# Optimization experiments

Measured on AMD Instinct MI355X. Metric: run time of the kernel, lower is better.

The kernel has to match this reference:

```python
import jax, jax.numpy as jnp
import numpy as np

V, C, H, L, T, B = 256, 1024, 16, 6, 1024, 8
HS = C // H
EPS = 1e-5


def setup_inputs() -> dict:
    key = jax.random.key(0)
    ks = jax.random.split(key, 20)
    s = 0.02
    inp = {
        "idx": jax.random.randint(ks[0], (B, T), 0, V),
        "tok_emb": jax.random.normal(ks[1], (V, C), jnp.float32) * s,
        "pos_emb": jax.random.normal(ks[2], (T, C), jnp.float32) * s,
        "Wq": jax.random.normal(ks[3], (L, C, C), jnp.float32) * s,
        "Wk": jax.random.normal(ks[4], (L, C, C), jnp.float32) * s,
        "Wv": jax.random.normal(ks[5], (L, C, C), jnp.float32) * s,
        "Wo": jax.random.normal(ks[6], (L, C, C), jnp.float32) * s,
        "bo": jnp.zeros((L, C), jnp.float32),
        "ln1_g": jnp.ones((L, C), jnp.float32),
        "ln1_b": jnp.zeros((L, C), jnp.float32),
        "ln2_g": jnp.ones((L, C), jnp.float32),
        "ln2_b": jnp.zeros((L, C), jnp.float32),
        "W1": jax.random.normal(ks[7], (L, C, 4 * C), jnp.float32) * s,
        "b1": jnp.zeros((L, 4 * C), jnp.float32),
        "W2": jax.random.normal(ks[8], (L, 4 * C, C), jnp.float32) * s,
        "b2": jnp.zeros((L, C), jnp.float32),
        "lnf_g": jnp.ones((C,), jnp.float32),
        "lnf_b": jnp.zeros((C,), jnp.float32),
        "Whead": jax.random.normal(ks[9], (C, V), jnp.float32) * s,
        "bhead": jnp.zeros((V,), jnp.float32),
    }
    return inp


def _ln(x, g, b):
    mu = jnp.mean(x, axis=-1, keepdims=True)
    var = jnp.mean(jnp.square(x - mu), axis=-1, keepdims=True)
    return (x - mu) * jax.lax.rsqrt(var + EPS) * g + b


def reference(idx, tok_emb, pos_emb, Wq, Wk, Wv, Wo, bo, ln1_g, ln1_b,
              ln2_g, ln2_b, W1, b1, W2, b2, lnf_g, lnf_b, Whead, bhead):
    Bv, Tv = idx.shape
    x = tok_emb[idx] + pos_emb[:Tv]  # [B,T,C]
    causal = jnp.tril(jnp.ones((Tv, Tv), bool))  # [T,T]
    scale = 1.0 / np.sqrt(HS)
    neg_inf = jnp.finfo(x.dtype).min
    for l in range(L):
        h = _ln(x, ln1_g[l], ln1_b[l])
        q = (h @ Wq[l]).reshape(Bv, Tv, H, HS)
        k = (h @ Wk[l]).reshape(Bv, Tv, H, HS)
        v = (h @ Wv[l]).reshape(Bv, Tv, H, HS)
        wei = jnp.einsum("bthd,bshd->bhts", q, k) * scale  # [B,H,T,T]
        wei = jnp.where(causal, wei, neg_inf)
        wei = jax.nn.softmax(wei, axis=-1)
        att = jnp.einsum("bhts,bshd->bthd", wei, v).reshape(Bv, Tv, C)
        x = x + att @ Wo[l] + bo[l]
        h2 = _ln(x, ln2_g[l], ln2_b[l])
        x = x + jax.nn.relu(h2 @ W1[l] + b1[l]) @ W2[l] + b2[l]
    x = _ln(x, lnf_g, lnf_b)
    logits = x @ Whead + bhead  # [B,T,V]
    return logits
```

## Files before the change

### kernel.cpp

```cpp
#include <hip/hip_runtime.h>

typedef unsigned short u16;
typedef unsigned int   u32;
typedef __attribute__((ext_vector_type(4))) float  f32x4;
typedef __attribute__((ext_vector_type(8))) __bf16 bf16x8;
typedef __attribute__((ext_vector_type(8))) short  s16x8;
typedef __attribute__((ext_vector_type(4))) unsigned short u16x4;

#define DEVFN __device__ __forceinline__

DEVFN float bf2f(u16 u) {
    u32 v = ((u32)u) << 16;
    return __builtin_bit_cast(float, v);
}
DEVFN u16 f2bf(float f) {
    u32 u = __builtin_bit_cast(u32, f);
    u32 r = u + 0x7FFFu + ((u >> 16) & 1u);
    return (u16)(r >> 16);
}

DEVFN void gload16(const void* g, void* l) {
    __builtin_amdgcn_global_load_lds(
        (const __attribute__((address_space(1))) void*)g,
        (__attribute__((address_space(3))) void*)l, 16, 0, 0);
}

__global__ __launch_bounds__(256) void embed_k(const int* __restrict__ idx,
                                               const float* __restrict__ tok,
                                               const float* __restrict__ pos,
                                               float* __restrict__ x)
{
    int i   = blockIdx.x * 256 + threadIdx.x;
    int row = i >> 8;
    int c   = (i & 255) << 2;
    int t   = row & 1023;
    int tk  = idx[row];
    float4 a = *(const float4*)&tok[(size_t)tk * 1024 + c];
    float4 p = *(const float4*)&pos[(size_t)t * 1024 + c];
    float4 r; r.x = a.x + p.x; r.y = a.y + p.y; r.z = a.z + p.z; r.w = a.w + p.w;
    *(float4*)&x[(size_t)row * 1024 + c] = r;
}

__global__ __launch_bounds__(256) void transpose_k(const float* __restrict__ W,
                                                   u16* __restrict__ Wt, int K, int N)
{
    __shared__ float tile[32][33];
    int n0 = blockIdx.x * 32, k0 = blockIdx.y * 32;
    int xx = threadIdx.x, ty = threadIdx.y;
#pragma unroll
    for (int yy = 0; yy < 4; ++yy) {
        int y = ty + yy * 8;
        tile[y][xx] = W[(size_t)(k0 + y) * N + n0 + xx];
    }
    __syncthreads();
#pragma unroll
    for (int yy = 0; yy < 4; ++yy) {
        int y = ty + yy * 8;
        Wt[(size_t)(n0 + y) * K + k0 + xx] = f2bf(tile[xx][y]);
    }
}

__global__ __launch_bounds__(256) void ln_k(const float* __restrict__ x,
                                            const float* __restrict__ g,
                                            const float* __restrict__ b,
                                            u16* __restrict__ out)
{
    const int row = blockIdx.x, tid = threadIdx.x;
    const float4 v = *(const float4*)&x[(size_t)row * 1024 + tid * 4];
    __shared__ float red[8];
    float s = v.x + v.y + v.z + v.w;
#pragma unroll
    for (int off = 32; off > 0; off >>= 1) s += __shfl_down(s, off);
    const int lane = tid & 63, wv = tid >> 6;
    if (lane == 0) red[wv] = s;
    __syncthreads();
    const float mu = (red[0] + red[1] + red[2] + red[3]) * (1.0f / 1024.0f);
    const float dx = v.x - mu, dy = v.y - mu, dz = v.z - mu, dw = v.w - mu;
    float s2 = dx * dx + dy * dy + dz * dz + dw * dw;
#pragma unroll
    for (int off = 32; off > 0; off >>= 1) s2 += __shfl_down(s2, off);
    if (lane == 0) red[4 + wv] = s2;
    __syncthreads();
    const float var = (red[4] + red[5] + red[6] + red[7]) * (1.0f / 1024.0f);
    const float rs  = rsqrtf(var + 1e-5f);
    const float4 gv = *(const float4*)&g[tid * 4];
    const float4 bv = *(const float4*)&b[tid * 4];
    u16x4 o;
    o.x = f2bf(dx * rs * gv.x + bv.x);
    o.y = f2bf(dy * rs * gv.y + bv.y);
    o.z = f2bf(dz * rs * gv.z + bv.z);
    o.w = f2bf(dw * rs * gv.w + bv.w);
    *(u16x4*)&out[(size_t)row * 1024 + tid * 4] = o;
}

template <int MODE>
__global__ __launch_bounds__(256) void gemm_bt(const u16* __restrict__ A,
                                               const u16* __restrict__ Bt,
                                               const float* __restrict__ bias,
                                               float* __restrict__ RES,
                                               u16* __restrict__ Ob,
                                               float* __restrict__ Of,
                                               int N, int K)
{
    __shared__ __align__(16) u16 As[128 * 32];
    __shared__ __align__(16) u16 Bs[128 * 32];
    const int tid  = threadIdx.x;
    const int lane = tid & 63, wave = tid >> 6;
    const int wr = wave >> 1, wc = wave & 1;
    const int l15 = lane & 15, l4 = lane >> 4;
    const int m0 = blockIdx.y * 128, n0 = blockIdx.x * 128;

    f32x4 acc[4][4];
    const f32x4 zz = {0.f, 0.f, 0.f, 0.f};
#pragma unroll
    for (int i = 0; i < 4; ++i)
#pragma unroll
        for (int j = 0; j < 4; ++j) acc[i][j] = zz;

    const int r0 = tid >> 2, q0q = (tid & 3) * 8;
    const int r1 = (tid + 256) >> 2, q1q = ((tid + 256) & 3) * 8;

    for (int k0 = 0; k0 < K; k0 += 32) {
        gload16(&A [(size_t)(m0 + r0) * K + k0 + q0q], &As[tid * 8]);
        gload16(&Bt[(size_t)(n0 + r0) * K + k0 + q0q], &Bs[tid * 8]);
        gload16(&A [(size_t)(m0 + r1) * K + k0 + q1q], &As[(tid + 256) * 8]);
        gload16(&Bt[(size_t)(n0 + r1) * K + k0 + q1q], &Bs[(tid + 256) * 8]);
        __syncthreads();
        s16x8 af[4], bw[4];
#pragma unroll
        for (int i = 0; i < 4; ++i)
            af[i] = *(const s16x8*)&As[(wr * 64 + i * 16 + l15) * 32 + l4 * 8];
#pragma unroll
        for (int j = 0; j < 4; ++j)
            bw[j] = *(const s16x8*)&Bs[(wc * 64 + j * 16 + l15) * 32 + l4 * 8];
#pragma unroll
        for (int i = 0; i < 4; ++i)
#pragma unroll
            for (int j = 0; j < 4; ++j)
                acc[i][j] = __builtin_amdgcn_mfma_f32_16x16x32_bf16(
                    __builtin_bit_cast(bf16x8, af[i]),
                    __builtin_bit_cast(bf16x8, bw[j]), acc[i][j], 0, 0, 0);
        __syncthreads();
    }

#pragma unroll
    for (int i = 0; i < 4; ++i) {
        const int rb = m0 + wr * 64 + i * 16 + l4 * 4;
#pragma unroll
        for (int j = 0; j < 4; ++j) {
            const int col = n0 + wc * 64 + j * 16 + l15;
            const float bval = (MODE == 0) ? 0.0f : bias[col];
#pragma unroll
            for (int r = 0; r < 4; ++r) {
                const size_t o = (size_t)(rb + r) * N + col;
                const float v = acc[i][j][r];
                if (MODE == 0)      Ob[o] = f2bf(v);
                else if (MODE == 1) RES[o] += v + bval;
                else if (MODE == 2) Ob[o] = f2bf(fmaxf(v + bval, 0.0f));
                else                Of[o] = v + bval;
            }
        }
    }
}

__global__ __launch_bounds__(256) void attn_mfma_k(const u16* __restrict__ QKV,
                                                   u16* __restrict__ Og)
{
    const int qt  = (int)(gridDim.x - 1 - blockIdx.x);
    const int bh  = blockIdx.y;
    const int b   = bh >> 4, h = bh & 15;
    const int tid = threadIdx.x;
    const int wq  = tid >> 6, lane = tid & 63;
    const int l15 = lane & 15, l4 = lane >> 4;

    __shared__ __align__(16) u16 Ks[64][72];
    __shared__ __align__(16) u16 Vt[64][72];
    __shared__ __align__(16) u16 Ps[4][16][68];
    u32* VtW = (u32*)&Vt[0][0];

    const int qrow0 = qt * 128 + wq * 32;

    const u16* Qbase = QKV + (size_t)b * 1024 * 3072 + h * 64;
    const u16* Kbase = Qbase + 1024;
    const u16* Vbase = Qbase + 2048;

    s16x8 aQ[2][2];
#pragma unroll
    for (int qi = 0; qi < 2; ++qi) {
        const u16* qsrc = Qbase + (size_t)(qrow0 + qi * 16 + l15) * 3072;
        aQ[qi][0] = *(const s16x8*)(qsrc + l4 * 8);
        aQ[qi][1] = *(const s16x8*)(qsrc + 32 + l4 * 8);
    }

    f32x4 O[2][4];
    const f32x4 zz = {0.f, 0.f, 0.f, 0.f};
    float mrow[2][4], lrow[2][4];
#pragma unroll
    for (int qi = 0; qi < 2; ++qi) {
#pragma unroll
        for (int dj = 0; dj < 4; ++dj) O[qi][dj] = zz;
#pragma unroll
        for (int r = 0; r < 4; ++r) { mrow[qi][r] = -3.0e38f; lrow[qi][r] = 0.f; }
    }

    const int srow = tid >> 3;
    const int soff = (tid & 7) * 8;
    const int vp   = tid >> 3;
    const int vdg  = tid & 7;

    const int ntiles = 2 * qt + 2;
    for (int t = 0; t < ntiles; ++t) {
        const int kv0 = t * 64;
        __syncthreads();
        {
            const u16* kb0 = Kbase + (size_t)(kv0 + srow) * 3072 + soff;
            *(s16x8*)&Ks[srow][soff]      = *(const s16x8*)kb0;
            *(s16x8*)&Ks[srow + 32][soff] = *(const s16x8*)(kb0 + (size_t)32 * 3072);
        }
        {
            const u16* vb0 = Vbase + (size_t)(kv0 + 2 * vp) * 3072 + vdg * 8;
            s16x8 v0 = *(const s16x8*)vb0;
            s16x8 v1 = *(const s16x8*)(vb0 + 3072);
#pragma unroll
            for (int e = 0; e < 8; ++e) {
                const int d = vdg * 8 + e;
                const int c = (vp + 4 * vdg) & 31;
                u32 pk = (u32)(u16)v0[e] | ((u32)(u16)v1[e] << 16);
                VtW[d * 36 + c] = pk;
            }
        }
        __syncthreads();

#pragma unroll
        for (int qi = 0; qi < 2; ++qi) {
            const int qlo = qrow0 + qi * 16;
            if (kv0 > qlo + 15) continue;
            f32x4 S[4];
#pragma unroll
            for (int kc = 0; kc < 4; ++kc) {
                f32x4 s = zz;
                s16x8 bK0 = *(const s16x8*)&Ks[kc * 16 + l15][l4 * 8];
                s16x8 bK1 = *(const s16x8*)&Ks[kc * 16 + l15][32 + l4 * 8];
                s = __builtin_amdgcn_mfma_f32_16x16x32_bf16(
                    __builtin_bit_cast(bf16x8, aQ[qi][0]), __builtin_bit_cast(bf16x8, bK0), s, 0, 0, 0);
                s = __builtin_amdgcn_mfma_f32_16x16x32_bf16(
                    __builtin_bit_cast(bf16x8, aQ[qi][1]), __builtin_bit_cast(bf16x8, bK1), s, 0, 0, 0);
#pragma unroll
                for (int r = 0; r < 4; ++r) S[kc][r] = s[r] * 0.125f;
            }
            if (kv0 + 63 > qlo) {
#pragma unroll
                for (int kc = 0; kc < 4; ++kc) {
                    const int k = kv0 + kc * 16 + l15;
#pragma unroll
                    for (int r = 0; r < 4; ++r)
                        if (k > qlo + l4 * 4 + r) S[kc][r] = -3.0e38f;
                }
            }
            float mloc[4];
#pragma unroll
            for (int r = 0; r < 4; ++r)
                mloc[r] = fmaxf(fmaxf(S[0][r], S[1][r]), fmaxf(S[2][r], S[3][r]));
#pragma unroll
            for (int off = 1; off < 16; off <<= 1)
#pragma unroll
                for (int r = 0; r < 4; ++r) mloc[r] = fmaxf(mloc[r], __shfl_xor(mloc[r], off));
            float alpha[4];
#pragma unroll
            for (int r = 0; r < 4; ++r) {
                const float mnew = fmaxf(mrow[qi][r], mloc[r]);
                alpha[r] = __expf(mrow[qi][r] - mnew);
                mrow[qi][r] = mnew;
            }
            float psum[4] = {0.f, 0.f, 0.f, 0.f};
#pragma unroll
            for (int kc = 0; kc < 4; ++kc)
#pragma unroll
                for (int r = 0; r < 4; ++r) {
                    const float p = __expf(S[kc][r] - mrow[qi][r]);
                    Ps[wq][l4 * 4 + r][kc * 16 + l15] = f2bf(p);
                    psum[r] += p;
                }
#pragma unroll
            for (int off = 1; off < 16; off <<= 1)
#pragma unroll
                for (int r = 0; r < 4; ++r) psum[r] += __shfl_xor(psum[r], off);
#pragma unroll
            for (int r = 0; r < 4; ++r) lrow[qi][r] = lrow[qi][r] * alpha[r] + psum[r];
#pragma unroll
            for (int dj = 0; dj < 4; ++dj)
#pragma unroll
                for (int r = 0; r < 4; ++r) O[qi][dj][r] *= alpha[r];
#pragma unroll
            for (int kk = 0; kk < 2; ++kk) {
                s16x8 aP = *(const s16x8*)&Ps[wq][l15][kk * 32 + l4 * 8];
#pragma unroll
                for (int dj = 0; dj < 4; ++dj) {
                    const int d = dj * 16 + l15;
                    const int c = (kk * 16 + l4 * 4 + 4 * ((d >> 3) & 7)) & 31;
                    s16x8 bV = *(const s16x8*)&VtW[d * 36 + c];
                    O[qi][dj] = __builtin_amdgcn_mfma_f32_16x16x32_bf16(
                        __builtin_bit_cast(bf16x8, aP), __builtin_bit_cast(bf16x8, bV),
                        O[qi][dj], 0, 0, 0);
                }
            }
        }
    }
#pragma unroll
    for (int qi = 0; qi < 2; ++qi)
#pragma unroll
        for (int dj = 0; dj < 4; ++dj)
#pragma unroll
            for (int r = 0; r < 4; ++r) {
                const size_t o = ((size_t)(b * 1024 + qrow0 + qi * 16 + l4 * 4 + r)) * 1024
                               + h * 64 + dj * 16 + l15;
                Og[o] = f2bf(O[qi][dj][r] / lrow[qi][r]);
            }
}

extern "C" void kernel_launch(void* const* d_in, const int* in_sizes, int n_in,
                              void* d_out, int out_size, void* d_ws, size_t ws_size,
                              hipStream_t stream)
{
    (void)in_sizes; (void)n_in; (void)out_size; (void)ws_size;
    const int*   idx  = (const int*)  d_in[0];
    const float* tok  = (const float*)d_in[1];
    const float* pos  = (const float*)d_in[2];
    const float* Wq   = (const float*)d_in[3];
    const float* Wk   = (const float*)d_in[4];
    const float* Wv   = (const float*)d_in[5];
    const float* Wo   = (const float*)d_in[6];
    const float* bo   = (const float*)d_in[7];
    const float* ln1g = (const float*)d_in[8];
    const float* ln1b = (const float*)d_in[9];
    const float* ln2g = (const float*)d_in[10];
    const float* ln2b = (const float*)d_in[11];
    const float* W1   = (const float*)d_in[12];
    const float* b1   = (const float*)d_in[13];
    const float* W2   = (const float*)d_in[14];
    const float* b2   = (const float*)d_in[15];
    const float* lnfg = (const float*)d_in[16];
    const float* lnfb = (const float*)d_in[17];
    const float* Wh   = (const float*)d_in[18];
    const float* bh   = (const float*)d_in[19];

    char* p = (char*)d_ws;
    float* x  = (float*)p; p += (size_t)8192 * 1024 * 4;
    u16* h    = (u16*)p;   p += (size_t)8192 * 1024 * 2;
    u16* qkv  = (u16*)p;   p += (size_t)8192 * 3072 * 2;
    u16* ab   = (u16*)p;   p += (size_t)8192 * 1024 * 2;
    u16* fb   = (u16*)p;   p += (size_t)8192 * 4096 * 2;
    u16* wqT  = (u16*)p;   p += (size_t)1024 * 1024 * 2;
    u16* wkT  = (u16*)p;   p += (size_t)1024 * 1024 * 2;
    u16* wvT  = (u16*)p;   p += (size_t)1024 * 1024 * 2;
    u16* woT  = (u16*)p;   p += (size_t)1024 * 1024 * 2;
    u16* w1T  = (u16*)p;   p += (size_t)1024 * 4096 * 2;
    u16* w2T  = (u16*)p;   p += (size_t)4096 * 1024 * 2;
    u16* whT  = (u16*)p;   p += (size_t)1024 * 256 * 2;

    const dim3 tb(32, 8);
    embed_k<<<8192, 256, 0, stream>>>(idx, tok, pos, x);
    for (int l = 0; l < 6; ++l) {
        transpose_k<<<dim3(32, 32),  tb, 0, stream>>>(Wq + (size_t)l * 1048576, wqT, 1024, 1024);
        transpose_k<<<dim3(32, 32),  tb, 0, stream>>>(Wk + (size_t)l * 1048576, wkT, 1024, 1024);
        transpose_k<<<dim3(32, 32),  tb, 0, stream>>>(Wv + (size_t)l * 1048576, wvT, 1024, 1024);
        transpose_k<<<dim3(32, 32),  tb, 0, stream>>>(Wo + (size_t)l * 1048576, woT, 1024, 1024);
        transpose_k<<<dim3(128, 32), tb, 0, stream>>>(W1 + (size_t)l * 4194304, w1T, 1024, 4096);
        transpose_k<<<dim3(32, 128), tb, 0, stream>>>(W2 + (size_t)l * 4194304, w2T, 4096, 1024);

        ln_k<<<8192, 256, 0, stream>>>(x, ln1g + l * 1024, ln1b + l * 1024, h);
        gemm_bt<0><<<dim3(24, 64), 256, 0, stream>>>(h, wqT, nullptr, nullptr, qkv, nullptr, 3072, 1024);
        attn_mfma_k<<<dim3(8, 128), 256, 0, stream>>>(qkv, ab);
        gemm_bt<1><<<dim3(8, 64),  256, 0, stream>>>(ab, woT, bo + l * 1024, x, nullptr, nullptr, 1024, 1024);
        ln_k<<<8192, 256, 0, stream>>>(x, ln2g + l * 1024, ln2b + l * 1024, h);
        gemm_bt<2><<<dim3(32, 64), 256, 0, stream>>>(h, w1T, b1 + l * 4096, nullptr, fb, nullptr, 4096, 1024);
        gemm_bt<1><<<dim3(8, 64),  256, 0, stream>>>(fb, w2T, b2 + l * 1024, x, nullptr, nullptr, 1024, 4096);
    }
    transpose_k<<<dim3(8, 32), tb, 0, stream>>>(Wh, whT, 1024, 256);
    ln_k<<<8192, 256, 0, stream>>>(x, lnfg, lnfb, h);
    gemm_bt<3><<<dim3(2, 64), 256, 0, stream>>>(h, whT, bh, nullptr, nullptr, (float*)d_out, 256, 1024);
}
```

Measured before the change: 2.949 ms.

## Double-buffer GEMM and attention LDS tiles, add XCD block swizzle

The GEMM now double-buffers its LDS tiles, prefetching the next K-slice with global_load_lds while the current one feeds MFMA, and uses one barrier per step instead of two. It also uses a 1D grid with an XCD-aware swizzle so neighbouring tiles land on the same chiplet's L2. The attention kernel prefetches the next K/V tile into registers, writes it to a second LDS buffer after compute, and raises wave priority around MFMA sections. Doubling LDS use may reduce occupancy, and the swizzle assumes the grid size is divisible by 8.

```diff
diff --git a/kernel.cpp b/kernel.cpp
--- a/kernel.cpp
+++ b/kernel.cpp
@@ -100,15 +100,19 @@
                                                float* __restrict__ RES,
                                                u16* __restrict__ Ob,
                                                float* __restrict__ Of,
-                                               int N, int K)
-{
-    __shared__ __align__(16) u16 As[128 * 32];
-    __shared__ __align__(16) u16 Bs[128 * 32];
+                                               int N, int K, int ntx)
+{
+    __shared__ __align__(16) u16 As[2][128 * 32];
+    __shared__ __align__(16) u16 Bs[2][128 * 32];
     const int tid  = threadIdx.x;
     const int lane = tid & 63, wave = tid >> 6;
     const int wr = wave >> 1, wc = wave & 1;
     const int l15 = lane & 15, l4 = lane >> 4;
-    const int m0 = blockIdx.y * 128, n0 = blockIdx.x * 128;
+
+    const int nwg = (int)gridDim.x;
+    const int bid = (int)blockIdx.x;
+    const int swz = (bid & 7) * (nwg >> 3) + (bid >> 3);
+    const int n0 = (swz % ntx) * 128, m0 = (swz / ntx) * 128;
 
     f32x4 acc[4][4];
     const f32x4 zz = {0.f, 0.f, 0.f, 0.f};
@@ -119,20 +123,34 @@
 
     const int r0 = tid >> 2, q0q = (tid & 3) * 8;
     const int r1 = (tid + 256) >> 2, q1q = ((tid + 256) & 3) * 8;
-
-    for (int k0 = 0; k0 < K; k0 += 32) {
-        gload16(&A [(size_t)(m0 + r0) * K + k0 + q0q], &As[tid * 8]);
-        gload16(&Bt[(size_t)(n0 + r0) * K + k0 + q0q], &Bs[tid * 8]);
-        gload16(&A [(size_t)(m0 + r1) * K + k0 + q1q], &As[(tid + 256) * 8]);
-        gload16(&Bt[(size_t)(n0 + r1) * K + k0 + q1q], &Bs[(tid + 256) * 8]);
-        __syncthreads();
+    const u16* Arow0 = &A [(size_t)(m0 + r0) * K + q0q];
+    const u16* Brow0 = &Bt[(size_t)(n0 + r0) * K + q0q];
+    const u16* Arow1 = &A [(size_t)(m0 + r1) * K + q1q];
+    const u16* Brow1 = &Bt[(size_t)(n0 + r1) * K + q1q];
+
+    gload16(Arow0, &As[0][tid * 8]);
+    gload16(Brow0, &Bs[0][tid * 8]);
+    gload16(Arow1, &As[0][(tid + 256) * 8]);
+    gload16(Brow1, &Bs[0][(tid + 256) * 8]);
+    __syncthreads();
+
+    const int S = K >> 5;
+    int cur = 0;
+    for (int s = 0; s < S; ++s) {
+        if (s + 1 < S) {
+            const int kn = (s + 1) << 5;
+            gload16(Arow0 + kn, &As[cur ^ 1][tid * 8]);
+            gload16(Brow0 + kn, &Bs[cur ^ 1][tid * 8]);
+            gload16(Arow1 + kn, &As[cur ^ 1][(tid + 256) * 8]);
+            gload16(Brow1 + kn, &Bs[cur ^ 1][(tid + 256) * 8]);
+        }
         s16x8 af[4], bw[4];
 #pragma unroll
         for (int i = 0; i < 4; ++i)
-            af[i] = *(const s16x8*)&As[(wr * 64 + i * 16 + l15) * 32 + l4 * 8];
+            af[i] = *(const s16x8*)&As[cur][(wr * 64 + i * 16 + l15) * 32 + l4 * 8];
 #pragma unroll
         for (int j = 0; j < 4; ++j)
-            bw[j] = *(const s16x8*)&Bs[(wc * 64 + j * 16 + l15) * 32 + l4 * 8];
+            bw[j] = *(const s16x8*)&Bs[cur][(wc * 64 + j * 16 + l15) * 32 + l4 * 8];
 #pragma unroll
         for (int i = 0; i < 4; ++i)
 #pragma unroll
@@ -141,6 +159,7 @@
                     __builtin_bit_cast(bf16x8, af[i]),
                     __builtin_bit_cast(bf16x8, bw[j]), acc[i][j], 0, 0, 0);
         __syncthreads();
+        cur ^= 1;
     }
 
 #pragma unroll
@@ -173,10 +192,9 @@
     const int wq  = tid >> 6, lane = tid & 63;
     const int l15 = lane & 15, l4 = lane >> 4;
 
-    __shared__ __align__(16) u16 Ks[64][72];
-    __shared__ __align__(16) u16 Vt[64][72];
+    __shared__ __align__(16) u16 Ks[2][64][72];
+    __shared__ __align__(16) u16 Vt[2][64][72];
     __shared__ __align__(16) u16 Ps[4][16][68];
-    u32* VtW = (u32*)&Vt[0][0];
 
     const int qrow0 = qt * 128 + wq * 32;
 
@@ -207,40 +225,54 @@
     const int soff = (tid & 7) * 8;
     const int vp   = tid >> 3;
     const int vdg  = tid & 7;
+    const int vc   = (vp + 4 * vdg) & 31;
 
     const int ntiles = 2 * qt + 2;
+    s16x8 kr0, kr1, vr0, vr1;
+
+    {
+        const u16* kb0 = Kbase + (size_t)srow * 3072 + soff;
+        kr0 = *(const s16x8*)kb0;
+        kr1 = *(const s16x8*)(kb0 + (size_t)32 * 3072);
+        const u16* vb0 = Vbase + (size_t)(2 * vp) * 3072 + vdg * 8;
+        vr0 = *(const s16x8*)vb0;
+        vr1 = *(const s16x8*)(vb0 + 3072);
+        *(s16x8*)&Ks[0][srow][soff]      = kr0;
+        *(s16x8*)&Ks[0][srow + 32][soff] = kr1;
+        u32* VtW = (u32*)&Vt[0][0][0];
+#pragma unroll
+        for (int e = 0; e < 8; ++e) {
+            u32 pk = (u32)(u16)vr0[e] | ((u32)(u16)vr1[e] << 16);
+            VtW[(vdg * 8 + e) * 36 + vc] = pk;
+        }
+    }
+    __syncthreads();
+
+    int cur = 0;
     for (int t = 0; t < ntiles; ++t) {
         const int kv0 = t * 64;
-        __syncthreads();
-        {
-            const u16* kb0 = Kbase + (size_t)(kv0 + srow) * 3072 + soff;
-            *(s16x8*)&Ks[srow][soff]      = *(const s16x8*)kb0;
-            *(s16x8*)&Ks[srow + 32][soff] = *(const s16x8*)(kb0 + (size_t)32 * 3072);
-        }
-        {
-            const u16* vb0 = Vbase + (size_t)(kv0 + 2 * vp) * 3072 + vdg * 8;
-            s16x8 v0 = *(const s16x8*)vb0;
-            s16x8 v1 = *(const s16x8*)(vb0 + 3072);
-#pragma unroll
-            for (int e = 0; e < 8; ++e) {
-                const int d = vdg * 8 + e;
-                const int c = (vp + 4 * vdg) & 31;
-                u32 pk = (u32)(u16)v0[e] | ((u32)(u16)v1[e] << 16);
-                VtW[d * 36 + c] = pk;
-            }
-        }
-        __syncthreads();
+        const bool more = (t + 1 < ntiles);
+        if (more) {
+            const u16* kb0 = Kbase + (size_t)(kv0 + 64 + srow) * 3072 + soff;
+            kr0 = *(const s16x8*)kb0;
+            kr1 = *(const s16x8*)(kb0 + (size_t)32 * 3072);
+            const u16* vb0 = Vbase + (size_t)(kv0 + 64 + 2 * vp) * 3072 + vdg * 8;
+            vr0 = *(const s16x8*)vb0;
+            vr1 = *(const s16x8*)(vb0 + 3072);
+        }
+        const u32* VtW = (const u32*)&Vt[cur][0][0];
 
 #pragma unroll
         for (int qi = 0; qi < 2; ++qi) {
             const int qlo = qrow0 + qi * 16;
             if (kv0 > qlo + 15) continue;
             f32x4 S[4];
+            __builtin_amdgcn_s_setprio(1);
 #pragma unroll
             for (int kc = 0; kc < 4; ++kc) {
                 f32x4 s = zz;
-                s16x8 bK0 = *(const s16x8*)&Ks[kc * 16 + l15][l4 * 8];
-                s16x8 bK1 = *(const s16x8*)&Ks[kc * 16 + l15][32 + l4 * 8];
+                s16x8 bK0 = *(const s16x8*)&Ks[cur][kc * 16 + l15][l4 * 8];
+                s16x8 bK1 = *(const s16x8*)&Ks[cur][kc * 16 + l15][32 + l4 * 8];
                 s = __builtin_amdgcn_mfma_f32_16x16x32_bf16(
                     __builtin_bit_cast(bf16x8, aQ[qi][0]), __builtin_bit_cast(bf16x8, bK0), s, 0, 0, 0);
                 s = __builtin_amdgcn_mfma_f32_16x16x32_bf16(
@@ -248,6 +280,7 @@
 #pragma unroll
                 for (int r = 0; r < 4; ++r) S[kc][r] = s[r] * 0.125f;
             }
+            __builtin_amdgcn_s_setprio(0);
             if (kv0 + 63 > qlo) {
 #pragma unroll
                 for (int kc = 0; kc < 4; ++kc) {
@@ -291,6 +324,7 @@
             for (int dj = 0; dj < 4; ++dj)
 #pragma unroll
                 for (int r = 0; r < 4; ++r) O[qi][dj][r] *= alpha[r];
+            __builtin_amdgcn_s_setprio(1);
 #pragma unroll
             for (int kk = 0; kk < 2; ++kk) {
                 s16x8 aP = *(const s16x8*)&Ps[wq][l15][kk * 32 + l4 * 8];
@@ -304,7 +338,21 @@
                         O[qi][dj], 0, 0, 0);
                 }
             }
-        }
+            __builtin_amdgcn_s_setprio(0);
+        }
+
+        if (more) {
+            *(s16x8*)&Ks[cur ^ 1][srow][soff]      = kr0;
+            *(s16x8*)&Ks[cur ^ 1][srow + 32][soff] = kr1;
+            u32* VtWn = (u32*)&Vt[cur ^ 1][0][0];
+#pragma unroll
+            for (int e = 0; e < 8; ++e) {
+                u32 pk = (u32)(u16)vr0[e] | ((u32)(u16)vr1[e] << 16);
+                VtWn[(vdg * 8 + e) * 36 + vc] = pk;
+            }
+        }
+        __syncthreads();
+        cur ^= 1;
     }
 #pragma unroll
     for (int qi = 0; qi < 2; ++qi)
@@ -369,14 +417,14 @@
         transpose_k<<<dim3(32, 128), tb, 0, stream>>>(W2 + (size_t)l * 4194304, w2T, 4096, 1024);
 
         ln_k<<<8192, 256, 0, stream>>>(x, ln1g + l * 1024, ln1b + l * 1024, h);
-        gemm_bt<0><<<dim3(24, 64), 256, 0, stream>>>(h, wqT, nullptr, nullptr, qkv, nullptr, 3072, 1024);
+        gemm_bt<0><<<1536, 256, 0, stream>>>(h, wqT, nullptr, nullptr, qkv, nullptr, 3072, 1024, 24);
         attn_mfma_k<<<dim3(8, 128), 256, 0, stream>>>(qkv, ab);
-        gemm_bt<1><<<dim3(8, 64),  256, 0, stream>>>(ab, woT, bo + l * 1024, x, nullptr, nullptr, 1024, 1024);
+        gemm_bt<1><<<512,  256, 0, stream>>>(ab, woT, bo + l * 1024, x, nullptr, nullptr, 1024, 1024, 8);
         ln_k<<<8192, 256, 0, stream>>>(x, ln2g + l * 1024, ln2b + l * 1024, h);
-        gemm_bt<2><<<dim3(32, 64), 256, 0, stream>>>(h, w1T, b1 + l * 4096, nullptr, fb, nullptr, 4096, 1024);
-        gemm_bt<1><<<dim3(8, 64),  256, 0, stream>>>(fb, w2T, b2 + l * 1024, x, nullptr, nullptr, 1024, 4096);
+        gemm_bt<2><<<2048, 256, 0, stream>>>(h, w1T, b1 + l * 4096, nullptr, fb, nullptr, 4096, 1024, 32);
+        gemm_bt<1><<<512,  256, 0, stream>>>(fb, w2T, b2 + l * 1024, x, nullptr, nullptr, 1024, 4096, 8);
     }
     transpose_k<<<dim3(8, 32), tb, 0, stream>>>(Wh, whT, 1024, 256);
     ln_k<<<8192, 256, 0, stream>>>(x, lnfg, lnfb, h);
-    gemm_bt<3><<<dim3(2, 64), 256, 0, stream>>>(h, whT, bh, nullptr, nullptr, (float*)d_out, 256, 1024);
-}
+    gemm_bt<3><<<128, 256, 0, stream>>>(h, whT, bh, nullptr, nullptr, (float*)d_out, 256, 1024, 2);
+}
```

Result: faster. 2.777 ms (-5.8%).

## Double-buffer GEMM with 256x128 tiles, swizzled block order, and attention MFMA priority

Applied to the files above, without the earlier changes.

The GEMM now uses a 256x128 output tile with each wave computing 128x64. It double-buffers the LDS staging so the next K-slice loads while MFMAs run on the current one, which removes one barrier per iteration. Launches become 1D grids with a grouped block-index swizzle to improve L2 reuse, and launch bounds request 2 blocks per CU. The attention kernel raises wave priority around its MFMA sections. The cost is more accumulator registers (128 floats per lane) and double the LDS, which may lower occupancy.

```diff
diff --git a/kernel.cpp b/kernel.cpp
--- a/kernel.cpp
+++ b/kernel.cpp
@@ -94,58 +94,82 @@
 }
 
 template <int MODE>
-__global__ __launch_bounds__(256) void gemm_bt(const u16* __restrict__ A,
-                                               const u16* __restrict__ Bt,
-                                               const float* __restrict__ bias,
-                                               float* __restrict__ RES,
-                                               u16* __restrict__ Ob,
-                                               float* __restrict__ Of,
-                                               int N, int K)
-{
-    __shared__ __align__(16) u16 As[128 * 32];
-    __shared__ __align__(16) u16 Bs[128 * 32];
+__global__ __launch_bounds__(256, 2) void gemm_bt(const u16* __restrict__ A,
+                                                  const u16* __restrict__ Bt,
+                                                  const float* __restrict__ bias,
+                                                  float* __restrict__ RES,
+                                                  u16* __restrict__ Ob,
+                                                  float* __restrict__ Of,
+                                                  int N, int K, int ntx)
+{
+    __shared__ __align__(16) u16 As[2][256 * 32];
+    __shared__ __align__(16) u16 Bs[2][128 * 32];
     const int tid  = threadIdx.x;
     const int lane = tid & 63, wave = tid >> 6;
     const int wr = wave >> 1, wc = wave & 1;
     const int l15 = lane & 15, l4 = lane >> 4;
-    const int m0 = blockIdx.y * 128, n0 = blockIdx.x * 128;
-
-    f32x4 acc[4][4];
+
+    const int nwg = (int)gridDim.x;
+    const int bid = (int)blockIdx.x;
+    const int swz = (bid & 7) * (nwg >> 3) + (bid >> 3);
+    const int n0 = (swz % ntx) * 128, m0 = (swz / ntx) * 256;
+
+    f32x4 acc[8][4];
     const f32x4 zz = {0.f, 0.f, 0.f, 0.f};
 #pragma unroll
-    for (int i = 0; i < 4; ++i)
+    for (int i = 0; i < 8; ++i)
 #pragma unroll
         for (int j = 0; j < 4; ++j) acc[i][j] = zz;
 
-    const int r0 = tid >> 2, q0q = (tid & 3) * 8;
-    const int r1 = (tid + 256) >> 2, q1q = ((tid + 256) & 3) * 8;
-
-    for (int k0 = 0; k0 < K; k0 += 32) {
-        gload16(&A [(size_t)(m0 + r0) * K + k0 + q0q], &As[tid * 8]);
-        gload16(&Bt[(size_t)(n0 + r0) * K + k0 + q0q], &Bs[tid * 8]);
-        gload16(&A [(size_t)(m0 + r1) * K + k0 + q1q], &As[(tid + 256) * 8]);
-        gload16(&Bt[(size_t)(n0 + r1) * K + k0 + q1q], &Bs[(tid + 256) * 8]);
-        __syncthreads();
-        s16x8 af[4], bw[4];
-#pragma unroll
-        for (int i = 0; i < 4; ++i)
-            af[i] = *(const s16x8*)&As[(wr * 64 + i * 16 + l15) * 32 + l4 * 8];
+    const u16* Ag[4];
+    const u16* Bg[2];
+#pragma unroll
+    for (int r = 0; r < 4; ++r) {
+        const int c = r * 256 + tid;
+        Ag[r] = &A[(size_t)(m0 + (c >> 2)) * K + (c & 3) * 8];
+    }
+#pragma unroll
+    for (int r = 0; r < 2; ++r) {
+        const int c = r * 256 + tid;
+        Bg[r] = &Bt[(size_t)(n0 + (c >> 2)) * K + (c & 3) * 8];
+    }
+
+#pragma unroll
+    for (int r = 0; r < 4; ++r) gload16(Ag[r], &As[0][(r * 256 + tid) * 8]);
+#pragma unroll
+    for (int r = 0; r < 2; ++r) gload16(Bg[r], &Bs[0][(r * 256 + tid) * 8]);
+    __syncthreads();
+
+    const int S = K >> 5;
+    int cur = 0;
+    for (int s = 0; s < S; ++s) {
+        if (s + 1 < S) {
+            const int kn = (s + 1) << 5;
+#pragma unroll
+            for (int r = 0; r < 4; ++r) gload16(Ag[r] + kn, &As[cur ^ 1][(r * 256 + tid) * 8]);
+#pragma unroll
+            for (int r = 0; r < 2; ++r) gload16(Bg[r] + kn, &Bs[cur ^ 1][(r * 256 + tid) * 8]);
+        }
+        s16x8 bw[4];
 #pragma unroll
         for (int j = 0; j < 4; ++j)
-            bw[j] = *(const s16x8*)&Bs[(wc * 64 + j * 16 + l15) * 32 + l4 * 8];
-#pragma unroll
-        for (int i = 0; i < 4; ++i)
+            bw[j] = *(const s16x8*)&Bs[cur][(wc * 64 + j * 16 + l15) * 32 + l4 * 8];
+#pragma unroll
+        for (int i = 0; i < 8; ++i) {
+            const s16x8 af = *(const s16x8*)&As[cur][(wr * 128 + i * 16 + l15) * 32 + l4 * 8];
 #pragma unroll
             for (int j = 0; j < 4; ++j)
                 acc[i][j] = __builtin_amdgcn_mfma_f32_16x16x32_bf16(
-                    __builtin_bit_cast(bf16x8, af[i]),
+                    __builtin_bit_cast(bf16x8, af),
                     __builtin_bit_cast(bf16x8, bw[j]), acc[i][j], 0, 0, 0);
+        }
         __syncthreads();
-    }
-
-#pragma unroll
-    for (int i = 0; i < 4; ++i) {
-        const int rb = m0 + wr * 64 + i * 16 + l4 * 4;
+        cur ^= 1;
+    }
+
+#pragma unroll
+    for (int i = 0; i < 8; ++i) {
+        const int rb = m0 + wr * 128 + i * 16 + l4 * 4;
 #pragma unroll
         for (int j = 0; j < 4; ++j) {
             const int col = n0 + wc * 64 + j * 16 + l15;
@@ -236,6 +260,7 @@
             const int qlo = qrow0 + qi * 16;
             if (kv0 > qlo + 15) continue;
             f32x4 S[4];
+            __builtin_amdgcn_s_setprio(1);
 #pragma unroll
             for (int kc = 0; kc < 4; ++kc) {
                 f32x4 s = zz;
@@ -248,6 +273,7 @@
 #pragma unroll
                 for (int r = 0; r < 4; ++r) S[kc][r] = s[r] * 0.125f;
             }
+            __builtin_amdgcn_s_setprio(0);
             if (kv0 + 63 > qlo) {
 #pragma unroll
                 for (int kc = 0; kc < 4; ++kc) {
@@ -291,6 +317,7 @@
             for (int dj = 0; dj < 4; ++dj)
 #pragma unroll
                 for (int r = 0; r < 4; ++r) O[qi][dj][r] *= alpha[r];
+            __builtin_amdgcn_s_setprio(1);
 #pragma unroll
             for (int kk = 0; kk < 2; ++kk) {
                 s16x8 aP = *(const s16x8*)&Ps[wq][l15][kk * 32 + l4 * 8];
@@ -304,6 +331,7 @@
                         O[qi][dj], 0, 0, 0);
                 }
             }
+            __builtin_amdgcn_s_setprio(0);
         }
     }
 #pragma unroll
@@ -369,14 +397,14 @@
         transpose_k<<<dim3(32, 128), tb, 0, stream>>>(W2 + (size_t)l * 4194304, w2T, 4096, 1024);
 
         ln_k<<<8192, 256, 0, stream>>>(x, ln1g + l * 1024, ln1b + l * 1024, h);
-        gemm_bt<0><<<dim3(24, 64), 256, 0, stream>>>(h, wqT, nullptr, nullptr, qkv, nullptr, 3072, 1024);
+        gemm_bt<0><<<768,  256, 0, stream>>>(h, wqT, nullptr, nullptr, qkv, nullptr, 3072, 1024, 24);
         attn_mfma_k<<<dim3(8, 128), 256, 0, stream>>>(qkv, ab);
-        gemm_bt<1><<<dim3(8, 64),  256, 0, stream>>>(ab, woT, bo + l * 1024, x, nullptr, nullptr, 1024, 1024);
+        gemm_bt<1><<<256,  256, 0, stream>>>(ab, woT, bo + l * 1024, x, nullptr, nullptr, 1024, 1024, 8);
         ln_k<<<8192, 256, 0, stream>>>(x, ln2g + l * 1024, ln2b + l * 1024, h);
-        gemm_bt<2><<<dim3(32, 64), 256, 0, stream>>>(h, w1T, b1 + l * 4096, nullptr, fb, nullptr, 4096, 1024);
-        gemm_bt<1><<<dim3(8, 64),  256, 0, stream>>>(fb, w2T, b2 + l * 1024, x, nullptr, nullptr, 1024, 4096);
+        gemm_bt<2><<<1024, 256, 0, stream>>>(h, w1T, b1 + l * 4096, nullptr, fb, nullptr, 4096, 1024, 32);
+        gemm_bt<1><<<256,  256, 0, stream>>>(fb, w2T, b2 + l * 1024, x, nullptr, nullptr, 1024, 4096, 8);
     }
     transpose_k<<<dim3(8, 32), tb, 0, stream>>>(Wh, whT, 1024, 256);
     ln_k<<<8192, 256, 0, stream>>>(x, lnfg, lnfb, h);
-    gemm_bt<3><<<dim3(2, 64), 256, 0, stream>>>(h, whT, bh, nullptr, nullptr, (float*)d_out, 256, 1024);
-}
+    gemm_bt<3><<<64, 256, 0, stream>>>(h, whT, bh, nullptr, nullptr, (float*)d_out, 256, 1024, 2);
+}
```

Result: slower. 3.190 ms (+8.2%).
